# Optimization experiments

Measured on AMD Instinct MI355X. Metric: run time of the kernel, lower is better.

Reference implementation:

```python
import jax, jax.numpy as jnp
import numpy as np

N_HEAD, D_HEAD, D_MODEL = 16, 64, 1024
QLEN, MEMLEN, BSZ = 1024, 1024, 2
KLEN = QLEN + MEMLEN  # rlen == klen
LN_EPS = 1e-5
NEG = -1e30


def _rel_shift(x):
    # x: [qlen, rlen, bsz, n_head] -> Transformer-XL relative shift
    q, r, b, n = x.shape
    zp = jnp.zeros((q, 1, b, n), x.dtype)
    xp = jnp.concatenate([zp, x], axis=1).reshape(r + 1, q, b, n)
    return xp[1:].reshape(q, r, b, n)


def _layer_norm(x, gamma, beta):
    mu = jnp.mean(x, axis=-1, keepdims=True)
    var = jnp.mean((x - mu) ** 2, axis=-1, keepdims=True)
    return (x - mu) * jax.lax.rsqrt(var + LN_EPS) * gamma + beta


def setup_inputs() -> dict:
    key = jax.random.key(0)
    ks = jax.random.split(key, 8)
    w = jax.random.normal(ks[0], (QLEN, BSZ, D_MODEL), jnp.float32)
    r = jax.random.normal(ks[1], (KLEN, D_MODEL), jnp.float32)
    r_w_bias = jax.random.normal(ks[2], (N_HEAD, D_HEAD), jnp.float32) * 0.02
    r_r_bias = jax.random.normal(ks[3], (N_HEAD, D_HEAD), jnp.float32) * 0.02
    mems = jax.random.normal(ks[4], (MEMLEN, BSZ, D_MODEL), jnp.float32)
    W_qkv = jax.random.normal(ks[5], (D_MODEL, 3 * N_HEAD * D_HEAD), jnp.float32) * 0.02
    W_r = jax.random.normal(ks[6], (D_MODEL, N_HEAD * D_HEAD), jnp.float32) * 0.02
    W_o = jax.random.normal(ks[7], (N_HEAD * D_HEAD, D_MODEL), jnp.float32) * 0.02
    ln_gamma = jnp.ones((D_MODEL,), jnp.float32)
    ln_beta = jnp.zeros((D_MODEL,), jnp.float32)
    # causal mask with memory: key j visible to query i iff j <= i + MEMLEN (True = keep)
    attn_mask = jnp.arange(KLEN)[None, :] <= (jnp.arange(QLEN)[:, None] + MEMLEN)
    return {"w": w, "r": r, "r_w_bias": r_w_bias, "r_r_bias": r_r_bias,
            "mems": mems, "attn_mask": attn_mask, "W_qkv": W_qkv, "W_r": W_r,
            "W_o": W_o, "ln_gamma": ln_gamma, "ln_beta": ln_beta}


def reference(w, r, r_w_bias, r_r_bias, mems, attn_mask, W_qkv, W_r, W_o, ln_gamma, ln_beta):
    qlen, bsz = w.shape[0], w.shape[1]
    scale = 1.0 / (D_HEAD ** 0.5)
    cat = jnp.concatenate([mems, w], axis=0)            # [klen, b, d_model]
    klen = cat.shape[0]
    w_heads = cat @ W_qkv                                # [klen, b, 3*H*D]
    r_head_k = (r @ W_r).reshape(-1, N_HEAD, D_HEAD)     # [rlen, H, D]
    w_head_q, w_head_k, w_head_v = jnp.split(w_heads, 3, axis=-1)
    w_head_q = w_head_q[-qlen:].reshape(qlen, bsz, N_HEAD, D_HEAD)
    w_head_k = w_head_k.reshape(klen, bsz, N_HEAD, D_HEAD)
    w_head_v = w_head_v.reshape(klen, bsz, N_HEAD, D_HEAD)
    AC = jnp.einsum('ibnd,jbnd->ijbn', w_head_q + r_w_bias, w_head_k)
    BD = jnp.einsum('ibnd,jnd->ijbn', w_head_q + r_r_bias, r_head_k)
    BD = _rel_shift(BD)
    attn_score = (AC + BD) * scale                       # [q, k, b, n]
    attn_score = jnp.where(attn_mask[:, :, None, None], attn_score, NEG)
    attn_prob = jax.nn.softmax(attn_score, axis=1)
    attn_vec = jnp.einsum('ijbn,jbnd->ibnd', attn_prob, w_head_v)
    attn_vec = attn_vec.reshape(qlen, bsz, N_HEAD * D_HEAD)
    attn_out = attn_vec @ W_o                            # [q, b, d_model]
    return _layer_norm(w + attn_out, ln_gamma, ln_beta)
```

## Files before the change

kernel.cpp:

```cpp
#include <hip/hip_runtime.h>
#include <hip/hip_bf16.h>

#define NHEAD 16
#define DHEAD 64
#define DMODEL 1024
#define QLEN 1024
#define MEMLEN 1024
#define BSZ 2
#define KLEN 2048
#define LN_EPS 1e-5f

typedef __hip_bfloat16 bf16;
typedef __attribute__((ext_vector_type(8))) short short8;
typedef __attribute__((ext_vector_type(4))) float f32x4;

__device__ __forceinline__ float b2f(bf16 x) { return __bfloat162float(x); }
__device__ __forceinline__ bf16 f2b(float x) { return __float2bfloat16(x); }
__device__ __forceinline__ short f2bs(float f) {
    bf16 h = __float2bfloat16(f);
    return *reinterpret_cast<short*>(&h);
}
__device__ __forceinline__ float s2f(short s) {
    bf16 h = *reinterpret_cast<bf16*>(&s);
    return __bfloat162float(h);
}

#define MFMA16(a, b, c) __builtin_amdgcn_mfma_f32_16x16x32_bf16(a, b, c, 0, 0, 0)

#define AS1 __attribute__((address_space(1)))
#define AS3 __attribute__((address_space(3)))
__device__ __forceinline__ void gld16(const bf16* g, bf16* l) {
    __builtin_amdgcn_global_load_lds((const AS1 void*)(uintptr_t)g,
                                     (AS3 void*)(uint32_t)(uintptr_t)l, 16, 0, 0);
}

__global__ __launch_bounds__(256)
void prep(const float* __restrict__ mems, const float* __restrict__ w,
          const float* __restrict__ r, const float* __restrict__ Wqkv,
          const float* __restrict__ Wr, const float* __restrict__ Wo,
          bf16* __restrict__ Abf, bf16* __restrict__ rbf,
          bf16* __restrict__ Wqkvt, bf16* __restrict__ Wrt,
          bf16* __restrict__ Wot) {
    __shared__ bf16 T[64][65];
    const int id = blockIdx.x;
    const int t = threadIdx.x;
    if (id < 6144) {
        const float* src;
        bf16* dst;
        int off;
        if (id < 2048)      { src = mems; dst = Abf;                       off = id; }
        else if (id < 4096) { src = w;    dst = Abf + (size_t)2048 * 1024; off = id - 2048; }
        else                { src = r;    dst = rbf;                       off = id - 4096; }
        int i = off * 256 + t;
        const float4 v = reinterpret_cast<const float4*>(src)[i];
        bf16 o[4] = {f2b(v.x), f2b(v.y), f2b(v.z), f2b(v.w)};
        reinterpret_cast<ulong1*>(dst)[i] = *reinterpret_cast<ulong1*>(o);
        return;
    }
    int tid2 = id - 6144;
    const float* in;
    bf16* out;
    int N, tn, tile;
    if (tid2 < 768)       { in = Wqkv; out = Wqkvt; N = 3072; tn = 48; tile = tid2; }
    else if (tid2 < 1024) { in = Wr;   out = Wrt;   N = 1024; tn = 16; tile = tid2 - 768; }
    else                  { in = Wo;   out = Wot;   N = 1024; tn = 16; tile = tid2 - 1024; }
    const int K = 1024;
    const int n0 = (tile % tn) * 64, k0 = (tile / tn) * 64;
    #pragma unroll
    for (int e = 0; e < 16; e++) {
        int flat = e * 256 + t;
        int kl = flat >> 6, nl = flat & 63;
        T[kl][nl] = f2b(in[(size_t)(k0 + kl) * N + n0 + nl]);
    }
    __syncthreads();
    #pragma unroll
    for (int e = 0; e < 16; e++) {
        int flat = e * 256 + t;
        int nl = flat >> 6, kl = flat & 63;
        out[(size_t)(n0 + nl) * K + k0 + kl] = T[kl][nl];
    }
}

__global__ __launch_bounds__(256)
void gemm_mfma(const bf16* __restrict__ A, const bf16* __restrict__ Bt,
               const bf16* __restrict__ A2, const bf16* __restrict__ B2,
               int M, int N, int K, int mode,
               const float* __restrict__ rwb, const float* __restrict__ rrb,
               bf16* __restrict__ Qw, bf16* __restrict__ Qr,
               bf16* __restrict__ Kb, bf16* __restrict__ Vt,
               bf16* __restrict__ Cb, float* __restrict__ Cf) {
    const int bm = blockIdx.x * 128, bn = blockIdx.y * 128;
    int sub = 0;
    const bf16* Ap = A;
    const bf16* Bp = Bt;
    if (mode == 0 && bm < 2048 && bn < 1024) { sub = 1; Ap = A2; Bp = B2; }
    __shared__ bf16 As[128 * 32];
    __shared__ bf16 Bs[128 * 32];
    const int t = threadIdx.x;
    const int w = t >> 6, lane = t & 63, quad = lane >> 4, l16 = lane & 15;
    const int wm = (w >> 1) * 64, wn = (w & 1) * 64;
    const int lrow = lane >> 2, lcol = (lane & 3) * 8;

    f32x4 acc[4][4];
    #pragma unroll
    for (int mt = 0; mt < 4; mt++)
        #pragma unroll
        for (int nt = 0; nt < 4; nt++) acc[mt][nt] = (f32x4){0.f, 0.f, 0.f, 0.f};

    for (int k0 = 0; k0 < K; k0 += 32) {
        #pragma unroll
        for (int e = 0; e < 2; e++) {
            int ch = w + 4 * e;
            int row = ch * 16 + lrow;
            gld16(Ap + (size_t)(bm + row) * K + k0 + lcol, As + ch * 512);
            gld16(Bp + (size_t)(bn + row) * K + k0 + lcol, Bs + ch * 512);
        }
        __syncthreads();
        short8 af[4], bfr[4];
        #pragma unroll
        for (int mt = 0; mt < 4; mt++)
            af[mt] = *reinterpret_cast<short8*>(&As[(wm + 16 * mt + l16) * 32 + quad * 8]);
        #pragma unroll
        for (int nt = 0; nt < 4; nt++)
            bfr[nt] = *reinterpret_cast<short8*>(&Bs[(wn + 16 * nt + l16) * 32 + quad * 8]);
        #pragma unroll
        for (int mt = 0; mt < 4; mt++)
            #pragma unroll
            for (int nt = 0; nt < 4; nt++)
                acc[mt][nt] = MFMA16(af[mt], bfr[nt], acc[mt][nt]);
        __syncthreads();
    }

    #pragma unroll
    for (int mt = 0; mt < 4; mt++)
        #pragma unroll
        for (int nt = 0; nt < 4; nt++)
            #pragma unroll
            for (int r = 0; r < 4; r++) {
                int m = bm + wm + 16 * mt + quad * 4 + r;
                int c = bn + wn + 16 * nt + l16;
                float v = acc[mt][nt][r];
                if (sub) {
                    Cb[(size_t)m * 1024 + c] = f2b(v);
                } else if (mode == 0) {
                    int seg = c >> 10, cc = c & 1023;
                    if (seg == 0) {
                        if (m >= 2048) {
                            size_t o = (size_t)(m - 2048) * 1024 + cc;
                            Qw[o] = f2b(v + rwb[cc]);
                            Qr[o] = f2b(v + rrb[cc]);
                        }
                    } else if (seg == 1) {
                        Kb[(size_t)m * 1024 + cc] = f2b(v);
                    } else {
                        Vt[((size_t)cc * 2 + (m & 1)) * 2048 + (m >> 1)] = f2b(v);
                    }
                } else {
                    Cf[(size_t)m * N + c] = v;
                }
            }
}

__global__ __launch_bounds__(256, 2)
void attn_mfma(const bf16* __restrict__ Qw, const bf16* __restrict__ Qr,
               const bf16* __restrict__ Kb, const bf16* __restrict__ Vt,
               const bf16* __restrict__ Rk, bf16* __restrict__ AVbf) {
    const int id = blockIdx.x;
    const int xcd = id & 7, local = id >> 3;
    int i0, pidx;
    if (local < 32) { i0 = local >> 1;              pidx = local & 1; }
    else            { i0 = 15 - ((local - 32) >> 1); pidx = 2 + (local & 1); }
    const int pair = xcd * 4 + pidx;
    const int b = pair & 1, n = pair >> 1;
    const int I0 = i0 * 64;

    const int tid = threadIdx.x;
    const int w = tid >> 6, lane = tid & 63;
    const int quad = lane >> 4, l16 = lane & 15;
    const int qbase = I0 + 16 * w;
    const int ln8 = lane >> 3;
    const int cs = (lane & 7) ^ (ln8 & 7);
    const int q0 = (quad ^ (l16 & 7)) * 8;
    const int q1 = q0 ^ 32;

    __shared__ bf16 Ks[2][64 * 64];
    __shared__ bf16 Vs[2][64 * 64];
    __shared__ bf16 Rs[3][64 * 64];
    __shared__ short WlB_s[4][16 * 80];
    __shared__ short Pb_s[4][16 * 72];
    short* WlB = WlB_s[w];
    short* Pb = Pb_s[w];

    short8 aqw[2], aqr[2];
    {
        const bf16* qp = Qw + ((size_t)(qbase + l16) * 2 + b) * 1024 + n * 64 + quad * 8;
        aqw[0] = *reinterpret_cast<const short8*>(qp);
        aqw[1] = *reinterpret_cast<const short8*>(qp + 32);
        const bf16* qp2 = Qr + ((size_t)(qbase + l16) * 2 + b) * 1024 + n * 64 + quad * 8;
        aqr[0] = *reinterpret_cast<const short8*>(qp2);
        aqr[1] = *reinterpret_cast<const short8*>(qp2 + 32);
    }

    f32x4 O[4];
    #pragma unroll
    for (int d = 0; d < 4; d++) O[d] = (f32x4){0.f, 0.f, 0.f, 0.f};
    float m_run = -1e30f;
    float pl[4] = {0.f, 0.f, 0.f, 0.f};

    const int T = i0 + 17;
    const int koff = b * 1024 + n * 64 + cs * 8;
    const size_t voff = (size_t)n * 262144 + b * 2048 + cs * 8;
    const int rcol = n * 64 + cs * 8;
    const int rbl = 48 - 16 * w;
    const int RB = 960 - I0;

    auto stageKV = [&](int tt) {
        const int J0 = tt * 64;
        bf16* kd = Ks[tt & 1];
        bf16* vd = Vs[tt & 1];
        #pragma unroll
        for (int e = 0; e < 2; e++) {
            int ch = w + 4 * e;
            int krow = J0 + ch * 8 + ln8;
            gld16(Kb + (size_t)krow * 2048 + koff, kd + ch * 512);
            int dl = ch * 8 + ln8;
            gld16(Vt + (size_t)dl * 4096 + voff + J0, vd + ch * 512);
        }
    };
    auto stageR = [&](int u) {
        bf16* rd = Rs[u % 3];
        #pragma unroll
        for (int e = 0; e < 2; e++) {
            int ch = w + 4 * e;
            int rrow = min(RB + u * 64 + ch * 8 + ln8, 2047);
            gld16(Rk + (size_t)rrow * 1024 + rcol, rd + ch * 512);
        }
    };

    stageKV(0); stageR(0); stageR(1);
    __syncthreads();

    for (int tt = 0; tt < T; tt++) {
        if (tt + 1 < T) { stageKV(tt + 1); stageR(tt + 2); }

        const bf16* K_ = Ks[tt & 1];
        const bf16* V_ = Vs[tt & 1];
        const bf16* R0 = Rs[tt % 3];
        const bf16* R1 = Rs[(tt + 1) % 3];
        const int J0 = tt * 64;

        #pragma unroll
        for (int s = 0; s < 5; s++) {
            int rb2 = rbl + 16 * s;
            const bf16* Rb = (rb2 & 64) ? R1 : R0;
            int rh = (rb2 & 63) + l16;
            short8 b0 = *reinterpret_cast<const short8*>(&Rb[rh * 64 + q0]);
            short8 b1 = *reinterpret_cast<const short8*>(&Rb[rh * 64 + q1]);
            f32x4 acc = (f32x4){0.f, 0.f, 0.f, 0.f};
            acc = MFMA16(aqr[0], b0, acc);
            acc = MFMA16(aqr[1], b1, acc);
            #pragma unroll
            for (int r = 0; r < 4; r++)
                WlB[(quad * 4 + r) * 80 + 16 * s + l16] = f2bs(acc[r]);
        }

        float sv[4][4];
        #pragma unroll
        for (int n16 = 0; n16 < 4; n16++) {
            int kr = 16 * n16 + l16;
            short8 k0 = *reinterpret_cast<const short8*>(&K_[kr * 64 + q0]);
            short8 k1 = *reinterpret_cast<const short8*>(&K_[kr * 64 + q1]);
            f32x4 acc = (f32x4){0.f, 0.f, 0.f, 0.f};
            acc = MFMA16(aqw[0], k0, acc);
            acc = MFMA16(aqw[1], k1, acc);
            #pragma unroll
            for (int r = 0; r < 4; r++) {
                int row = quad * 4 + r, col = 16 * n16 + l16;
                float s = (acc[r] + s2f(WlB[row * 80 + col - row + 15])) * 0.125f;
                if (J0 + col > qbase + row + MEMLEN) s = -1e30f;
                sv[n16][r] = s;
            }
        }

        float mx = sv[0][0];
        #pragma unroll
        for (int n16 = 0; n16 < 4; n16++)
            #pragma unroll
            for (int r = 0; r < 4; r++) mx = fmaxf(mx, sv[n16][r]);
        #pragma unroll
        for (int msk = 1; msk < 16; msk <<= 1) mx = fmaxf(mx, __shfl_xor(mx, msk));
        if (mx > m_run + 8.f) {
            const float alpha = __expf(m_run - mx);
            m_run = mx;
            #pragma unroll
            for (int r = 0; r < 4; r++) pl[r] *= alpha;
            #pragma unroll
            for (int d = 0; d < 4; d++)
                #pragma unroll
                for (int r = 0; r < 4; r++) O[d][r] *= alpha;
        }
        #pragma unroll
        for (int n16 = 0; n16 < 4; n16++)
            #pragma unroll
            for (int r = 0; r < 4; r++) sv[n16][r] = __expf(sv[n16][r] - m_run);
        #pragma unroll
        for (int r = 0; r < 4; r++)
            pl[r] += sv[0][r] + sv[1][r] + sv[2][r] + sv[3][r];

        #pragma unroll
        for (int n16 = 0; n16 < 4; n16++)
            #pragma unroll
            for (int r = 0; r < 4; r++)
                Pb[(quad * 4 + r) * 72 + 16 * n16 + l16] = f2bs(sv[n16][r]);
        short8 ap0 = *reinterpret_cast<short8*>(&Pb[l16 * 72 + quad * 8]);
        short8 ap1 = *reinterpret_cast<short8*>(&Pb[l16 * 72 + 32 + quad * 8]);

        #pragma unroll
        for (int ds = 0; ds < 4; ds++) {
            int dr = 16 * ds + l16;
            short8 v0 = *reinterpret_cast<const short8*>(&V_[dr * 64 + q0]);
            short8 v1 = *reinterpret_cast<const short8*>(&V_[dr * 64 + q1]);
            O[ds] = MFMA16(ap0, v0, O[ds]);
            O[ds] = MFMA16(ap1, v1, O[ds]);
        }

        __syncthreads();
    }

    float lr[4];
    #pragma unroll
    for (int r = 0; r < 4; r++) {
        float s = pl[r];
        #pragma unroll
        for (int msk = 1; msk < 16; msk <<= 1) s += __shfl_xor(s, msk);
        lr[r] = s;
    }
    #pragma unroll
    for (int ds = 0; ds < 4; ds++)
        #pragma unroll
        for (int r = 0; r < 4; r++) {
            int q = qbase + quad * 4 + r;
            AVbf[((size_t)q * 2 + b) * 1024 + n * 64 + 16 * ds + l16] =
                f2b(O[ds][r] / lr[r]);
        }
}

__global__ __launch_bounds__(256)
void ln_res(const float* __restrict__ ao, const float* __restrict__ w,
            const float* __restrict__ gamma, const float* __restrict__ beta,
            float* __restrict__ out) {
    const int m = blockIdx.x;
    const int t = threadIdx.x;
    __shared__ float red[256];
    float x[4];
    #pragma unroll
    for (int e = 0; e < 4; e++) {
        int c = e * 256 + t;
        x[e] = ao[(size_t)m * DMODEL + c] + w[(size_t)m * DMODEL + c];
    }
    float s = x[0] + x[1] + x[2] + x[3];
    red[t] = s;
    __syncthreads();
    #pragma unroll
    for (int off = 128; off; off >>= 1) {
        if (t < off) red[t] += red[t + off];
        __syncthreads();
    }
    const float mu = red[0] * (1.f / 1024.f);
    __syncthreads();
    float s2 = 0.f;
    #pragma unroll
    for (int e = 0; e < 4; e++) { float dx = x[e] - mu; s2 += dx * dx; }
    red[t] = s2;
    __syncthreads();
    #pragma unroll
    for (int off = 128; off; off >>= 1) {
        if (t < off) red[t] += red[t + off];
        __syncthreads();
    }
    const float rstd = rsqrtf(red[0] * (1.f / 1024.f) + LN_EPS);
    #pragma unroll
    for (int e = 0; e < 4; e++) {
        int c = e * 256 + t;
        out[(size_t)m * DMODEL + c] = (x[e] - mu) * rstd * gamma[c] + beta[c];
    }
}

extern "C" void kernel_launch(void* const* d_in, const int* in_sizes, int n_in,
                              void* d_out, int out_size, void* d_ws, size_t ws_size,
                              hipStream_t stream) {
    const float* w        = (const float*)d_in[0];
    const float* r        = (const float*)d_in[1];
    const float* r_w_bias = (const float*)d_in[2];
    const float* r_r_bias = (const float*)d_in[3];
    const float* mems     = (const float*)d_in[4];
    const float* W_qkv    = (const float*)d_in[6];
    const float* W_r      = (const float*)d_in[7];
    const float* W_o      = (const float*)d_in[8];
    const float* gamma    = (const float*)d_in[9];
    const float* beta     = (const float*)d_in[10];
    float* out = (float*)d_out;

    bf16* Abf    = (bf16*)d_ws;
    bf16* Wqkvt  = Abf   + (size_t)4096 * 1024;
    bf16* Wrt    = Wqkvt + (size_t)3072 * 1024;
    bf16* Wot    = Wrt   + (size_t)1024 * 1024;
    bf16* rbf    = Wot   + (size_t)1024 * 1024;
    bf16* Qw     = rbf   + (size_t)2048 * 1024;
    bf16* Qr     = Qw    + (size_t)2048 * 1024;
    bf16* Kb     = Qr    + (size_t)2048 * 1024;
    bf16* Vt     = Kb    + (size_t)4096 * 1024;
    bf16* Rk     = Vt    + (size_t)2048 * 2048;
    bf16* AVbf   = Rk    + (size_t)2048 * 1024;
    float* attn_out = (float*)Abf;

    dim3 b256(256);
    prep<<<dim3(7424), b256, 0, stream>>>(mems, w, r, W_qkv, W_r, W_o,
                                          Abf, rbf, Wqkvt, Wrt, Wot);
    gemm_mfma<<<dim3(32, 24), b256, 0, stream>>>(
        Abf, Wqkvt, rbf, Wrt, 4096, 3072, 1024, 0, r_w_bias, r_r_bias,
        Qw, Qr, Kb, Vt, Rk, nullptr);
    attn_mfma<<<dim3(512), b256, 0, stream>>>(Qw, Qr, Kb, Vt, Rk, AVbf);
    gemm_mfma<<<dim3(16, 8), b256, 0, stream>>>(
        AVbf, Wot, nullptr, nullptr, 2048, 1024, 1024, 2, nullptr, nullptr,
        nullptr, nullptr, nullptr, nullptr, nullptr, attn_out);
    ln_res<<<dim3(QLEN * BSZ), b256, 0, stream>>>(attn_out, w, gamma, beta, out);
}
```

Baseline: 259.0 us.

## Split attention KV range into two halves and merge with combine kernel

The attention kernel now splits each query tile's key loop into two halves run by separate blocks, doubling the grid to 1024 blocks. Each block writes fp32 partial outputs plus its running max and sum, and a new combine kernel merges them into the bf16 attention vector. Shared-memory buffering is cut from double/triple to single/double so three blocks can share a CU, and MFMA sections get raised wave priority. The cost is an extra kernel launch, extra partial-output traffic, and less overlap because loads are now followed directly by a barrier.

```diff
diff --git a/kernel.cpp b/kernel.cpp
--- a/kernel.cpp
+++ b/kernel.cpp
@@ -161,18 +161,25 @@
             }
 }
 
-__global__ __launch_bounds__(256, 2)
+__global__ __launch_bounds__(256, 3)
 void attn_mfma(const bf16* __restrict__ Qw, const bf16* __restrict__ Qr,
                const bf16* __restrict__ Kb, const bf16* __restrict__ Vt,
-               const bf16* __restrict__ Rk, bf16* __restrict__ AVbf) {
+               const bf16* __restrict__ Rk, float* __restrict__ Opart0,
+               float* __restrict__ Opart1, float2* __restrict__ ML) {
     const int id = blockIdx.x;
     const int xcd = id & 7, local = id >> 3;
-    int i0, pidx;
-    if (local < 32) { i0 = local >> 1;              pidx = local & 1; }
-    else            { i0 = 15 - ((local - 32) >> 1); pidx = 2 + (local & 1); }
+    const int quarter = local >> 5, idx = local & 31;
+    const int a = idx >> 1, p = idx & 1;
+    int i0, pidx, half;
+    if (quarter < 2) { i0 = a;      pidx = p;     half = quarter; }
+    else             { i0 = 15 - a; pidx = 2 + p; half = quarter - 2; }
     const int pair = xcd * 4 + pidx;
     const int b = pair & 1, n = pair >> 1;
     const int I0 = i0 * 64;
+    const int T = i0 + 17;
+    const int h0 = (T + 1) >> 1;
+    const int t_beg = half ? h0 : 0;
+    const int t_end = half ? T : h0;
 
     const int tid = threadIdx.x;
     const int w = tid >> 6, lane = tid & 63;
@@ -183,9 +190,9 @@
     const int q0 = (quad ^ (l16 & 7)) * 8;
     const int q1 = q0 ^ 32;
 
-    __shared__ bf16 Ks[2][64 * 64];
-    __shared__ bf16 Vs[2][64 * 64];
-    __shared__ bf16 Rs[3][64 * 64];
+    __shared__ bf16 Ks[64 * 64];
+    __shared__ bf16 Vs[64 * 64];
+    __shared__ bf16 Rs[2][64 * 64];
     __shared__ short WlB_s[4][16 * 80];
     __shared__ short Pb_s[4][16 * 72];
     short* WlB = WlB_s[w];
@@ -207,7 +214,6 @@
     float m_run = -1e30f;
     float pl[4] = {0.f, 0.f, 0.f, 0.f};
 
-    const int T = i0 + 17;
     const int koff = b * 1024 + n * 64 + cs * 8;
     const size_t voff = (size_t)n * 262144 + b * 2048 + cs * 8;
     const int rcol = n * 64 + cs * 8;
@@ -216,19 +222,17 @@
 
     auto stageKV = [&](int tt) {
         const int J0 = tt * 64;
-        bf16* kd = Ks[tt & 1];
-        bf16* vd = Vs[tt & 1];
         #pragma unroll
         for (int e = 0; e < 2; e++) {
             int ch = w + 4 * e;
             int krow = J0 + ch * 8 + ln8;
-            gld16(Kb + (size_t)krow * 2048 + koff, kd + ch * 512);
+            gld16(Kb + (size_t)krow * 2048 + koff, Ks + ch * 512);
             int dl = ch * 8 + ln8;
-            gld16(Vt + (size_t)dl * 4096 + voff + J0, vd + ch * 512);
+            gld16(Vt + (size_t)dl * 4096 + voff + J0, Vs + ch * 512);
         }
     };
     auto stageR = [&](int u) {
-        bf16* rd = Rs[u % 3];
+        bf16* rd = Rs[u & 1];
         #pragma unroll
         for (int e = 0; e < 2; e++) {
             int ch = w + 4 * e;
@@ -237,16 +241,15 @@
         }
     };
 
-    stageKV(0); stageR(0); stageR(1);
-    __syncthreads();
-
-    for (int tt = 0; tt < T; tt++) {
-        if (tt + 1 < T) { stageKV(tt + 1); stageR(tt + 2); }
-
-        const bf16* K_ = Ks[tt & 1];
-        const bf16* V_ = Vs[tt & 1];
-        const bf16* R0 = Rs[tt % 3];
-        const bf16* R1 = Rs[(tt + 1) % 3];
+    stageR(t_beg);
+
+    for (int tt = t_beg; tt < t_end; tt++) {
+        stageKV(tt);
+        stageR(tt + 1);
+        __syncthreads();
+
+        const bf16* R0 = Rs[tt & 1];
+        const bf16* R1 = Rs[(tt + 1) & 1];
         const int J0 = tt * 64;
 
         #pragma unroll
@@ -257,8 +260,10 @@
             short8 b0 = *reinterpret_cast<const short8*>(&Rb[rh * 64 + q0]);
             short8 b1 = *reinterpret_cast<const short8*>(&Rb[rh * 64 + q1]);
             f32x4 acc = (f32x4){0.f, 0.f, 0.f, 0.f};
+            __builtin_amdgcn_s_setprio(1);
             acc = MFMA16(aqr[0], b0, acc);
             acc = MFMA16(aqr[1], b1, acc);
+            __builtin_amdgcn_s_setprio(0);
             #pragma unroll
             for (int r = 0; r < 4; r++)
                 WlB[(quad * 4 + r) * 80 + 16 * s + l16] = f2bs(acc[r]);
@@ -268,11 +273,13 @@
         #pragma unroll
         for (int n16 = 0; n16 < 4; n16++) {
             int kr = 16 * n16 + l16;
-            short8 k0 = *reinterpret_cast<const short8*>(&K_[kr * 64 + q0]);
-            short8 k1 = *reinterpret_cast<const short8*>(&K_[kr * 64 + q1]);
+            short8 k0 = *reinterpret_cast<const short8*>(&Ks[kr * 64 + q0]);
+            short8 k1 = *reinterpret_cast<const short8*>(&Ks[kr * 64 + q1]);
             f32x4 acc = (f32x4){0.f, 0.f, 0.f, 0.f};
+            __builtin_amdgcn_s_setprio(1);
             acc = MFMA16(aqw[0], k0, acc);
             acc = MFMA16(aqw[1], k1, acc);
+            __builtin_amdgcn_s_setprio(0);
             #pragma unroll
             for (int r = 0; r < 4; r++) {
                 int row = quad * 4 + r, col = 16 * n16 + l16;
@@ -315,14 +322,16 @@
         short8 ap0 = *reinterpret_cast<short8*>(&Pb[l16 * 72 + quad * 8]);
         short8 ap1 = *reinterpret_cast<short8*>(&Pb[l16 * 72 + 32 + quad * 8]);
 
+        __builtin_amdgcn_s_setprio(1);
         #pragma unroll
         for (int ds = 0; ds < 4; ds++) {
             int dr = 16 * ds + l16;
-            short8 v0 = *reinterpret_cast<const short8*>(&V_[dr * 64 + q0]);
-            short8 v1 = *reinterpret_cast<const short8*>(&V_[dr * 64 + q1]);
+            short8 v0 = *reinterpret_cast<const short8*>(&Vs[dr * 64 + q0]);
+            short8 v1 = *reinterpret_cast<const short8*>(&Vs[dr * 64 + q1]);
             O[ds] = MFMA16(ap0, v0, O[ds]);
             O[ds] = MFMA16(ap1, v1, O[ds]);
         }
+        __builtin_amdgcn_s_setprio(0);
 
         __syncthreads();
     }
@@ -335,14 +344,44 @@
         for (int msk = 1; msk < 16; msk <<= 1) s += __shfl_xor(s, msk);
         lr[r] = s;
     }
-    #pragma unroll
-    for (int ds = 0; ds < 4; ds++)
+    if (l16 == 0) {
         #pragma unroll
         for (int r = 0; r < 4; r++) {
             int q = qbase + quad * 4 + r;
-            AVbf[((size_t)q * 2 + b) * 1024 + n * 64 + 16 * ds + l16] =
-                f2b(O[ds][r] / lr[r]);
-        }
+            ML[(size_t)half * 32768 + (q * 2 + b) * 16 + n] =
+                make_float2(m_run, lr[r]);
+        }
+    }
+    float* Od = half ? Opart1 : Opart0;
+    #pragma unroll
+    for (int ds = 0; ds < 4; ds++)
+        #pragma unroll
+        for (int r = 0; r < 4; r++) {
+            int q = qbase + quad * 4 + r;
+            Od[((size_t)q * 2 + b) * 1024 + n * 64 + 16 * ds + l16] =
+                O[ds][r] / lr[r];
+        }
+}
+
+__global__ __launch_bounds__(256)
+void attn_combine(const float* __restrict__ O0, const float* __restrict__ O1,
+                  const float2* __restrict__ ML, bf16* __restrict__ AVbf) {
+    const int row = blockIdx.x;
+    const int t = threadIdx.x;
+    const int n = t >> 4;
+    const float2 a0 = ML[row * 16 + n];
+    const float2 a1 = ML[32768 + row * 16 + n];
+    const float m = fmaxf(a0.x, a1.x);
+    float w0 = a0.y * __expf(a0.x - m);
+    float w1 = a1.y * __expf(a1.x - m);
+    const float inv = 1.f / (w0 + w1);
+    w0 *= inv; w1 *= inv;
+    const f32x4 p0 = reinterpret_cast<const f32x4*>(O0)[row * 256 + t];
+    const f32x4 p1 = reinterpret_cast<const f32x4*>(O1)[row * 256 + t];
+    short o[4];
+    #pragma unroll
+    for (int j = 0; j < 4; j++) o[j] = f2bs(p0[j] * w0 + p1[j] * w1);
+    reinterpret_cast<ulong1*>(AVbf)[row * 256 + t] = *reinterpret_cast<ulong1*>(o);
 }
 
 __global__ __launch_bounds__(256)
@@ -413,6 +452,9 @@
     bf16* Rk     = Vt    + (size_t)2048 * 2048;
     bf16* AVbf   = Rk    + (size_t)2048 * 1024;
     float* attn_out = (float*)Abf;
+    float* Opart0   = (float*)Abf;
+    float* Opart1   = (float*)Wqkvt;
+    float2* ML      = (float2*)rbf;
 
     dim3 b256(256);
     prep<<<dim3(7424), b256, 0, stream>>>(mems, w, r, W_qkv, W_r, W_o,
@@ -420,7 +462,9 @@
     gemm_mfma<<<dim3(32, 24), b256, 0, stream>>>(
         Abf, Wqkvt, rbf, Wrt, 4096, 3072, 1024, 0, r_w_bias, r_r_bias,
         Qw, Qr, Kb, Vt, Rk, nullptr);
-    attn_mfma<<<dim3(512), b256, 0, stream>>>(Qw, Qr, Kb, Vt, Rk, AVbf);
+    attn_mfma<<<dim3(1024), b256, 0, stream>>>(Qw, Qr, Kb, Vt, Rk,
+                                               Opart0, Opart1, ML);
+    attn_combine<<<dim3(2048), b256, 0, stream>>>(Opart0, Opart1, ML, AVbf);
     gemm_mfma<<<dim3(16, 8), b256, 0, stream>>>(
         AVbf, Wot, nullptr, nullptr, 2048, 1024, 1024, 2, nullptr, nullptr,
         nullptr, nullptr, nullptr, nullptr, nullptr, attn_out);
```

New measurement: 262.6 us. No clear change (+1.4%).
